# Kernel tuning notes

Hardware: AMD Instinct MI355X
Metric: run time of the kernel (lower is better)

Reference implementation:

```python
import jax, jax.numpy as jnp
import numpy as np
from jax import lax

EPS = 1e-5  # BatchNorm eps (torch default)


def _bn_relu_conv3x3_s2(x, bn_w, bn_b, bn_m, bn_v, w, b):
    # eval-mode BatchNorm2d -> ReLU -> conv3x3 stride 2 pad 1 (NCHW)
    inv = bn_w / jnp.sqrt(bn_v + EPS)
    y = x * inv[None, :, None, None] + (bn_b - bn_m * inv)[None, :, None, None]
    y = jax.nn.relu(y)
    y = lax.conv_general_dilated(y, w, window_strides=(2, 2),
                                 padding=((1, 1), (1, 1)),
                                 dimension_numbers=("NCHW", "OIHW", "NCHW"))
    return y + b[None, :, None, None]


def _avgpool2x2(x):
    B, C, H, W = x.shape
    return x.reshape(B, C, H // 2, 2, W // 2, 2).mean(axis=(3, 5))


def setup_inputs() -> dict:
    key = jax.random.key(0)
    ks = jax.random.split(key, 24)
    C, C3 = 128, 128 // 3
    d = {"x": jax.random.normal(ks[0], (8, C, 96, 96), jnp.float32)}
    for i, p in enumerate(["f", "g", "h"]):
        base = 1 + i * 6
        d[p + "_bn_w"] = jax.random.uniform(ks[base], (C,), jnp.float32, 0.5, 1.5)
        d[p + "_bn_b"] = jax.random.normal(ks[base + 1], (C,), jnp.float32) * 0.1
        d[p + "_bn_m"] = jax.random.normal(ks[base + 2], (C,), jnp.float32) * 0.1
        d[p + "_bn_v"] = jax.random.uniform(ks[base + 3], (C,), jnp.float32, 0.5, 1.5)
        d[p + "_w"] = jax.random.normal(ks[base + 4], (C, C, 3, 3), jnp.float32) * (1.0 / np.sqrt(9 * C))
        d[p + "_b"] = jax.random.normal(ks[base + 5], (C,), jnp.float32) * 0.01
    d["se_cw"] = jax.random.normal(ks[19], (C3, 2 * C), jnp.float32) * (1.0 / np.sqrt(2 * C))
    d["se_cb"] = jax.random.normal(ks[20], (C3,), jnp.float32) * 0.01
    d["se_uw"] = jax.random.normal(ks[21], (C, C3), jnp.float32) * (1.0 / np.sqrt(C3))
    d["se_ub"] = jax.random.normal(ks[22], (C,), jnp.float32) * 0.01
    d["gamma"] = jax.random.normal(ks[23], (1,), jnp.float32) * 0.5
    return d


def reference(x, f_bn_w, f_bn_b, f_bn_m, f_bn_v, f_w, f_b,
              g_bn_w, g_bn_b, g_bn_m, g_bn_v, g_w, g_b,
              h_bn_w, h_bn_b, h_bn_m, h_bn_v, h_w, h_b,
              se_cw, se_cb, se_uw, se_ub, gamma):
    B, C, H, W = x.shape
    left = _avgpool2x2(x)  # isPrimary=False branch -> [B,C,H/2,W/2]

    f = _bn_relu_conv3x3_s2(x, f_bn_w, f_bn_b, f_bn_m, f_bn_v, f_w, f_b)
    g = _bn_relu_conv3x3_s2(x, g_bn_w, g_bn_b, g_bn_m, g_bn_v, g_w, g_b)
    h = _bn_relu_conv3x3_s2(x, h_bn_w, h_bn_b, h_bn_m, h_bn_v, h_w, h_b)

    Ho, Wo = f.shape[2], f.shape[3]
    N = Ho * Wo
    ff = f.reshape(B, C, N)
    gg = g.reshape(B, C, N)
    hh = h.reshape(B, C, N)

    # s = softmax over last axis of f^T g : [B, N, N]
    scores = jnp.einsum("bcn,bcm->bnm", ff, gg)
    attn = jax.nn.softmax(scores, axis=2)
    s = jnp.einsum("bcn,bnm->bcm", hh, attn).reshape(B, C, Ho, Wo)
    s = gamma[0] * s

    # CompetitiveSE: global-avg x and s -> concat(2C) -> ReLU/1x1(C//3) -> ReLU/1x1(C)
    wx = x.mean(axis=(2, 3))          # [B, C]
    ws = s.mean(axis=(2, 3))          # [B, C]
    wcat = jnp.concatenate([wx, ws], axis=1)  # [B, 2C]
    se = jax.nn.relu(wcat) @ se_cw.T + se_cb
    se = jax.nn.relu(se) @ se_uw.T + se_ub    # [B, C]

    return (left + s) * (1.0 + se[:, :, None, None])
```

## Files before the change

kernel.cpp:

```cpp
#include <hip/hip_runtime.h>
#include <hip/hip_bf16.h>

#define B_   8
#define C_   128
#define H_   96
#define W_   96
#define HP_  98
#define HO_  48
#define N_   2304
#define K_CONV 1152
#define PLANE_IN  9216
#define TOT_OUT (B_*C_*N_)

typedef __attribute__((ext_vector_type(8))) short          s16x8;
typedef __attribute__((ext_vector_type(8))) unsigned short u16x8;
typedef __attribute__((ext_vector_type(4))) unsigned short u16x4;
typedef __attribute__((ext_vector_type(4))) float          f32x4;

#define SW(row, q)   (((row) << 6) + ((((q) ^ (((row) >> 1) & 3))) << 4))
#define SW8(row, q)  (((row) << 7) + ((((q) ^ ((row) & 7))) << 4))
#define SW16(row, q) (((row) << 8) + ((((q) ^ ((row) & 15))) << 4))

__device__ __forceinline__ ushort f2bf(float f) {
  __hip_bfloat16 h = __float2bfloat16(f);
  return *reinterpret_cast<ushort*>(&h);
}

__device__ __forceinline__ float block_reduce_sum_256(float v) {
  #pragma unroll
  for (int o = 32; o > 0; o >>= 1) v += __shfl_down(v, o, 64);
  __shared__ float r[4];
  int lane = threadIdx.x & 63, wv = threadIdx.x >> 6;
  if (lane == 0) r[wv] = v;
  __syncthreads();
  float s = 0.f;
  if (threadIdx.x == 0) s = r[0] + r[1] + r[2] + r[3];
  __syncthreads();
  return s;
}

__global__ void k_prep(const float* __restrict__ w0, const float* __restrict__ b0,
                       const float* __restrict__ m0, const float* __restrict__ v0,
                       const float* __restrict__ w1, const float* __restrict__ b1,
                       const float* __restrict__ m1, const float* __restrict__ v1,
                       const float* __restrict__ w2, const float* __restrict__ b2,
                       const float* __restrict__ m2, const float* __restrict__ v2,
                       float* __restrict__ inv, float* __restrict__ beta) {
  int p = blockIdx.x, c = threadIdx.x;
  const float* w = (p == 0 ? w0 : p == 1 ? w1 : w2);
  const float* bb = (p == 0 ? b0 : p == 1 ? b1 : b2);
  const float* m = (p == 0 ? m0 : p == 1 ? m1 : m2);
  const float* v = (p == 0 ? v0 : p == 1 ? v1 : v2);
  if (c < C_) {
    float iv = w[c] / sqrtf(v[c] + 1e-5f);
    inv[p * 128 + c] = iv;
    beta[p * 128 + c] = bb[c] - m[c] * iv;
  }
}

__global__ __launch_bounds__(256) void k_prep_w(const float* __restrict__ w0,
                                                const float* __restrict__ w1,
                                                const float* __restrict__ w2,
                                                ushort* __restrict__ o0,
                                                ushort* __restrict__ o1,
                                                ushort* __restrict__ o2) {
  int p = blockIdx.y;
  const float* w = (p == 0 ? w0 : p == 1 ? w1 : w2);
  ushort* wb = (p == 0 ? o0 : p == 1 ? o1 : o2);
  int id = blockIdx.x * 256 + threadIdx.x;
  if (id >= C_ * K_CONV) return;
  int co = id / K_CONV, rem = id - co * K_CONV;
  int tap = rem >> 7, ci = rem & 127;
  wb[id] = f2bf(w[co * K_CONV + ci * 9 + tap]);
}

__global__ __launch_bounds__(256) void k_prep_y(const float* __restrict__ x,
                                                const float* __restrict__ pinv,
                                                const float* __restrict__ pbeta,
                                                ushort* __restrict__ y0,
                                                ushort* __restrict__ y1,
                                                ushort* __restrict__ y2) {
  const int h1 = blockIdx.x, b = blockIdx.y, t = threadIdx.x;
  ushort* ys[3] = {y0 + (size_t)b * HP_ * HP_ * C_,
                   y1 + (size_t)b * HP_ * HP_ * C_,
                   y2 + (size_t)b * HP_ * HP_ * C_};
  u16x8 zer = (u16x8)0;
  if (h1 == 0 || h1 == HP_ - 1) {
    for (int p = 0; p < 3; ++p)
      for (int g = t; g < HP_ * C_ / 8; g += 256)
        *(u16x8*)(ys[p] + (size_t)h1 * HP_ * C_ + g * 8) = zer;
    return;
  }
  __shared__ float xs[128][97];
  const int h = h1 - 1;
  const float* xb = x + (size_t)b * C_ * PLANE_IN + h * W_;
  for (int id = t; id < 128 * 24; id += 256) {
    int ci = id / 24, w4 = id - ci * 24;
    float4 v = *(const float4*)(xb + (size_t)ci * PLANE_IN + w4 * 4);
    xs[ci][w4 * 4 + 0] = v.x; xs[ci][w4 * 4 + 1] = v.y;
    xs[ci][w4 * 4 + 2] = v.z; xs[ci][w4 * 4 + 3] = v.w;
  }
  __syncthreads();
  if (t < 32) {
    int side = t >> 4, cg = t & 15;
    for (int p = 0; p < 3; ++p)
      *(u16x8*)(ys[p] + ((size_t)h1 * HP_ + (side ? HP_ - 1 : 0)) * C_ + cg * 8) = zer;
  }
  for (int p = 0; p < 3; ++p) {
    const float* inv = pinv + p * 128;
    const float* bet = pbeta + p * 128;
    for (int g = t; g < 96 * 16; g += 256) {
      int wdx = g >> 4, cg = g & 15;
      u16x8 o;
      #pragma unroll
      for (int k = 0; k < 8; ++k) {
        int ci = cg * 8 + k;
        o[k] = f2bf(fmaxf(xs[ci][wdx] * inv[ci] + bet[ci], 0.f));
      }
      *(u16x8*)(ys[p] + ((size_t)h1 * HP_ + (wdx + 1)) * C_ + cg * 8) = o;
    }
  }
}

__global__ __launch_bounds__(256) void k_meanx(const float* __restrict__ x,
                                               float* __restrict__ wcat) {
  int bc = blockIdx.x;
  const float* p = x + (size_t)bc * PLANE_IN;
  float s = 0.f;
  for (int i = threadIdx.x; i < PLANE_IN; i += 256) s += p[i];
  s = block_reduce_sum_256(s);
  if (threadIdx.x == 0) {
    int b = bc >> 7, c = bc & 127;
    wcat[b * 256 + c] = fmaxf(s * (1.f / PLANE_IN), 0.f);
  }
}

__global__ __launch_bounds__(256) void k_conv3(
    const ushort* __restrict__ y0, const ushort* __restrict__ y1, const ushort* __restrict__ y2,
    const ushort* __restrict__ w0, const ushort* __restrict__ w1, const ushort* __restrict__ w2,
    const float* __restrict__ bi0, const float* __restrict__ bi1, const float* __restrict__ bi2,
    ushort* __restrict__ fo, ushort* __restrict__ go, ushort* __restrict__ ho) {
  __shared__ __align__(16) char smem[16384];
  char* As = smem;
  char* Bs = smem + 8192;
  const int br = blockIdx.y, b = blockIdx.z, n0 = blockIdx.x * 64;
  const int t = threadIdx.x, l = t & 63, w = t >> 6;
  const ushort* yb = (br == 0 ? y0 : br == 1 ? y1 : y2) + (size_t)b * HP_ * HP_ * C_;
  const ushort* wb = (br == 0 ? w0 : br == 1 ? w1 : w2);
  const float* bias = (br == 0 ? bi0 : br == 1 ? bi1 : bi2);
  const int pos = t >> 2, q = t & 3;
  const int n_glob = n0 + pos;
  const int oh = n_glob / HO_, ow = n_glob - oh * HO_;
  const int mh = (w & 1) * 64, nh = (w >> 1) * 32;
  f32x4 acc[4][2];
  #pragma unroll
  for (int i = 0; i < 4; ++i)
    #pragma unroll
    for (int j = 0; j < 2; ++j) acc[i][j] = (f32x4)0.f;

  for (int k0 = 0; k0 < K_CONV; k0 += 32) {
    int tap = k0 >> 7, ci0 = k0 & 127;
    int kh = tap / 3, kw = tap - kh * 3;
    #pragma unroll
    for (int g2 = 0; g2 < 2; ++g2) {
      int g = t + g2 * 256, row = g >> 2, qq = g & 3;
      u16x8 d = *(const u16x8*)(wb + row * K_CONV + k0 + qq * 8);
      *(u16x8*)(As + SW(row, qq)) = d;
    }
    {
      int h1 = 2 * oh + kh, w1 = 2 * ow + kw;
      u16x8 d = *(const u16x8*)(yb + ((size_t)h1 * HP_ + w1) * C_ + ci0 + q * 8);
      *(u16x8*)(Bs + SW(pos, q)) = d;
    }
    __syncthreads();
    s16x8 af[4], bf[2];
    #pragma unroll
    for (int i = 0; i < 4; ++i) {
      int r = mh + i * 16 + (l & 15);
      af[i] = *(const s16x8*)(As + SW(r, (l >> 4)));
    }
    #pragma unroll
    for (int j = 0; j < 2; ++j) {
      int r = nh + j * 16 + (l & 15);
      bf[j] = *(const s16x8*)(Bs + SW(r, (l >> 4)));
    }
    #pragma unroll
    for (int i = 0; i < 4; ++i)
      #pragma unroll
      for (int j = 0; j < 2; ++j)
        acc[i][j] = __builtin_amdgcn_mfma_f32_16x16x32_bf16(af[i], bf[j], acc[i][j], 0, 0, 0);
    __syncthreads();
  }

  if (br < 2) {
    ushort* out = (br == 0) ? fo : go;
    ushort* tb = (ushort*)smem;
    #pragma unroll
    for (int i = 0; i < 4; ++i) {
      int co4 = mh + i * 16 + (l >> 4) * 4;
      float4 bi = *(const float4*)&bias[co4];
      float bia[4] = {bi.x, bi.y, bi.z, bi.w};
      #pragma unroll
      for (int j = 0; j < 2; ++j) {
        int pp = nh + j * 16 + (l & 15);
        #pragma unroll
        for (int r = 0; r < 4; ++r)
          tb[pp * 128 + co4 + r] = f2bf(acc[i][j][r] + bia[r]);
      }
    }
    __syncthreads();
    #pragma unroll
    for (int it = 0; it < 4; ++it) {
      int g = t + it * 256;
      int row = g >> 4, gg = g & 15;
      u16x8 d = *(const u16x8*)(tb + row * 128 + gg * 8);
      *(u16x8*)(out + ((size_t)b * N_ + n0 + row) * C_ + gg * 8) = d;
    }
  } else {
    ushort* tb = (ushort*)smem;
    #pragma unroll
    for (int i = 0; i < 4; ++i) {
      int co4 = mh + i * 16 + (l >> 4) * 4;
      float4 bi = *(const float4*)&bias[co4];
      float bia[4] = {bi.x, bi.y, bi.z, bi.w};
      #pragma unroll
      for (int j = 0; j < 2; ++j) {
        int pp = nh + j * 16 + (l & 15);
        #pragma unroll
        for (int r = 0; r < 4; ++r)
          tb[(co4 + r) * 64 + pp] = f2bf(acc[i][j][r] + bia[r]);
      }
    }
    __syncthreads();
    for (int g = t; g < 1024; g += 256) {
      int co = g >> 3, off2 = (g & 7) * 8;
      u16x8 d = *(const u16x8*)(tb + co * 64 + off2);
      *(u16x8*)(ho + ((size_t)b * C_ + co) * N_ + n0 + off2) = d;
    }
  }
}

__global__ __launch_bounds__(256) void k_stats(const ushort* __restrict__ f,
                                               const ushort* __restrict__ g,
                                               float2* __restrict__ pstats) {
  __shared__ __align__(16) char smem[32768];
  char* fs = smem;
  char* gs = smem + 16384;
  const int blk = blockIdx.x;
  const int b = blk & 7, t2 = blk >> 3;
  const int n0 = (t2 % 36) * 64, mz = t2 / 36;
  const int t = threadIdx.x, l = t & 63, w = t >> 6, lo = l & 15, quad = l >> 4;
  const ushort* fb = f + (size_t)b * N_ * C_;
  const ushort* gb = g + (size_t)b * N_ * C_;
  #pragma unroll
  for (int it = 0; it < 4; ++it) {
    int G = t + it * 256, row = G >> 4, g16 = G & 15;
    *(u16x8*)(fs + SW16(row, g16)) = *(const u16x8*)(fb + (size_t)(n0 + row) * C_ + g16 * 8);
  }
  __syncthreads();
  s16x8 af[4];
  #pragma unroll
  for (int ks = 0; ks < 4; ++ks)
    af[ks] = *(const s16x8*)(fs + SW16(w * 16 + lo, ks * 4 + quad));
  float mloc[4], lloc[4];
  #pragma unroll
  for (int r = 0; r < 4; ++r) { mloc[r] = -1e30f; lloc[r] = 0.f; }
  const int m_beg = mz * 576;

  for (int i9 = 0; i9 < 9; ++i9) {
    int m0 = m_beg + i9 * 64;
    __syncthreads();
    #pragma unroll
    for (int it = 0; it < 4; ++it) {
      int G = t + it * 256, row = G >> 4, g16 = G & 15;
      *(u16x8*)(gs + SW16(row, g16)) = *(const u16x8*)(gb + (size_t)(m0 + row) * C_ + g16 * 8);
    }
    __syncthreads();
    f32x4 acc[4];
    #pragma unroll
    for (int j = 0; j < 4; ++j) acc[j] = (f32x4)0.f;
    #pragma unroll
    for (int ks = 0; ks < 4; ++ks)
      #pragma unroll
      for (int j = 0; j < 4; ++j) {
        s16x8 bf = *(const s16x8*)(gs + SW16(j * 16 + lo, ks * 4 + quad));
        acc[j] = __builtin_amdgcn_mfma_f32_16x16x32_bf16(af[ks], bf, acc[j], 0, 0, 0);
      }
    #pragma unroll
    for (int r = 0; r < 4; ++r) {
      float vmax = fmaxf(fmaxf(acc[0][r], acc[1][r]), fmaxf(acc[2][r], acc[3][r]));
      float mn = fmaxf(mloc[r], vmax);
      lloc[r] = lloc[r] * __expf(mloc[r] - mn) +
                __expf(acc[0][r] - mn) + __expf(acc[1][r] - mn) +
                __expf(acc[2][r] - mn) + __expf(acc[3][r] - mn);
      mloc[r] = mn;
    }
  }
  #pragma unroll
  for (int r = 0; r < 4; ++r) {
    #pragma unroll
    for (int o = 1; o < 16; o <<= 1) {
      float mo = __shfl_xor(mloc[r], o, 64);
      float lo2 = __shfl_xor(lloc[r], o, 64);
      float mn = fmaxf(mloc[r], mo);
      lloc[r] = lloc[r] * __expf(mloc[r] - mn) + lo2 * __expf(mo - mn);
      mloc[r] = mn;
    }
  }
  if (lo == 0) {
    #pragma unroll
    for (int r = 0; r < 4; ++r)
      pstats[((size_t)mz * B_ + b) * N_ + n0 + w * 16 + quad * 4 + r] =
          make_float2(mloc[r], lloc[r]);
  }
}

__global__ __launch_bounds__(256) void k_stats_red(const float2* __restrict__ p,
                                                   float2* __restrict__ stats) {
  int idx = blockIdx.x * 256 + threadIdx.x;
  if (idx >= B_ * N_) return;
  float mx = -1e30f, ls = 0.f;
  #pragma unroll
  for (int z = 0; z < 4; ++z) {
    float2 s = p[(size_t)z * B_ * N_ + idx];
    float mn = fmaxf(mx, s.x);
    ls = ls * __expf(mx - mn) + s.y * __expf(s.x - mn);
    mx = mn;
  }
  stats[idx] = make_float2(mx, ls);
}

__global__ __launch_bounds__(256) void k_attn_out(const ushort* __restrict__ f,
                                                  const ushort* __restrict__ g,
                                                  const ushort* __restrict__ h,
                                                  const float2* __restrict__ stats,
                                                  float* __restrict__ spart) {
  __shared__ __align__(16) char smem[35072];
  char* gs = smem;
  char* pTb = smem + 16384;
  const int blk = blockIdx.x;
  const int b = blk & 7, t2 = blk >> 3;
  const int m0 = (t2 % 36) * 64, nz = t2 / 36;
  const int t = threadIdx.x, l = t & 63, w = t >> 6, lo = l & 15, quad = l >> 4;
  const ushort* fb = f + (size_t)b * N_ * C_;
  const ushort* gb = g + (size_t)b * N_ * C_;
  const ushort* hb = h + (size_t)b * C_ * N_;
  const float2* stb = stats + (size_t)b * N_;
  #pragma unroll
  for (int it = 0; it < 4; ++it) {
    int G = t + it * 256, row = G >> 4, g16 = G & 15;
    *(u16x8*)(gs + SW16(row, g16)) = *(const u16x8*)(gb + (size_t)(m0 + row) * C_ + g16 * 8);
  }
  __syncthreads();
  f32x4 accs[2][4];
  #pragma unroll
  for (int i = 0; i < 2; ++i)
    #pragma unroll
    for (int j = 0; j < 4; ++j) accs[i][j] = (f32x4)0.f;
  const int n_beg = nz * 576;

  for (int i9 = 0; i9 < 9; ++i9) {
    int nb = n_beg + i9 * 64;
    char* pT = pTb + ((i9 & 1) << 13);
    s16x8 af[4], ah[2][2];
    #pragma unroll
    for (int ks = 0; ks < 4; ++ks)
      af[ks] = *(const s16x8*)(fb + (size_t)(nb + w * 16 + lo) * C_ + (ks * 4 + quad) * 8);
    #pragma unroll
    for (int i = 0; i < 2; ++i)
      #pragma unroll
      for (int ks = 0; ks < 2; ++ks)
        ah[i][ks] = *(const s16x8*)(hb + (size_t)((2 * w + i) * 16 + lo) * N_ + nb + (ks * 4 + quad) * 8);
    f32x4 sc[4];
    #pragma unroll
    for (int j = 0; j < 4; ++j) sc[j] = (f32x4)0.f;
    #pragma unroll
    for (int ks = 0; ks < 4; ++ks)
      #pragma unroll
      for (int j = 0; j < 4; ++j) {
        s16x8 bg = *(const s16x8*)(gs + SW16(j * 16 + lo, ks * 4 + quad));
        sc[j] = __builtin_amdgcn_mfma_f32_16x16x32_bf16(af[ks], bg, sc[j], 0, 0, 0);
      }
    float mxr[4], ilr[4];
    #pragma unroll
    for (int r = 0; r < 4; ++r) {
      float2 st = stb[nb + w * 16 + quad * 4 + r];
      mxr[r] = st.x; ilr[r] = 1.f / st.y;
    }
    const int nl = w * 16 + quad * 4;
    #pragma unroll
    for (int j = 0; j < 4; ++j) {
      u16x4 pv;
      #pragma unroll
      for (int r = 0; r < 4; ++r)
        pv[r] = f2bf(__expf(sc[j][r] - mxr[r]) * ilr[r]);
      *(u16x4*)(pT + SW8(j * 16 + lo, nl >> 3) + (nl & 7) * 2) = pv;
    }
    __syncthreads();
    #pragma unroll
    for (int ks = 0; ks < 2; ++ks)
      #pragma unroll
      for (int j = 0; j < 4; ++j) {
        s16x8 bp = *(const s16x8*)(pT + SW8(j * 16 + lo, ks * 4 + quad));
        accs[0][j] = __builtin_amdgcn_mfma_f32_16x16x32_bf16(ah[0][ks], bp, accs[0][j], 0, 0, 0);
        accs[1][j] = __builtin_amdgcn_mfma_f32_16x16x32_bf16(ah[1][ks], bp, accs[1][j], 0, 0, 0);
      }
  }
  __syncthreads();
  float* ss = (float*)smem;
  #pragma unroll
  for (int i = 0; i < 2; ++i) {
    int c0 = (2 * w + i) * 16 + quad * 4;
    #pragma unroll
    for (int j = 0; j < 4; ++j) {
      int m = j * 16 + lo;
      #pragma unroll
      for (int r = 0; r < 4; ++r)
        ss[(c0 + r) * 68 + m] = accs[i][j][r];
    }
  }
  __syncthreads();
  float* outp = spart + (size_t)nz * TOT_OUT + (size_t)b * C_ * N_ + m0;
  #pragma unroll
  for (int it = 0; it < 8; ++it) {
    int idx = t + it * 256;
    int c = idx >> 4, mq = idx & 15;
    float4 v = *(const float4*)&ss[c * 68 + mq * 4];
    *(float4*)&outp[(size_t)c * N_ + mq * 4] = v;
  }
}

__global__ __launch_bounds__(256) void k_sred(const float* __restrict__ spart,
                                              const float* __restrict__ gammap,
                                              float* __restrict__ sbuf) {
  int idx = blockIdx.x * 256 + threadIdx.x;
  if (idx >= TOT_OUT) return;
  float s = spart[idx] + spart[(size_t)TOT_OUT + idx] +
            spart[2 * (size_t)TOT_OUT + idx] + spart[3 * (size_t)TOT_OUT + idx];
  sbuf[idx] = gammap[0] * s;
}

__global__ __launch_bounds__(256) void k_means(const float* __restrict__ s,
                                               float* __restrict__ wcat) {
  int bc = blockIdx.x;
  const float* p = s + (size_t)bc * N_;
  float sm = 0.f;
  for (int i = threadIdx.x; i < N_; i += 256) sm += p[i];
  sm = block_reduce_sum_256(sm);
  if (threadIdx.x == 0) {
    int b = bc >> 7, c = bc & 127;
    wcat[b * 256 + 128 + c] = fmaxf(sm * (1.f / N_), 0.f);
  }
}

__global__ __launch_bounds__(128) void k_se(const float* __restrict__ wcat,
                                            const float* __restrict__ cw,
                                            const float* __restrict__ cb,
                                            const float* __restrict__ uw,
                                            const float* __restrict__ ub,
                                            float* __restrict__ se) {
  const int b = blockIdx.x, t = threadIdx.x;
  __shared__ float wc[256];
  __shared__ float s1[42];
  wc[t] = wcat[b * 256 + t];
  wc[128 + t] = wcat[b * 256 + 128 + t];
  __syncthreads();
  if (t < 42) {
    float a = cb[t];
    const float* r = cw + (size_t)t * 256;
    for (int k = 0; k < 256; ++k) a += wc[k] * r[k];
    s1[t] = fmaxf(a, 0.f);
  }
  __syncthreads();
  {
    float a = ub[t];
    const float* r = uw + (size_t)t * 42;
    for (int j = 0; j < 42; ++j) a += s1[j] * r[j];
    se[b * 128 + t] = a;
  }
}

__global__ __launch_bounds__(256) void k_final(const float* __restrict__ x,
                                               const float* __restrict__ s,
                                               const float* __restrict__ se,
                                               float* __restrict__ out) {
  int idx = blockIdx.x * 256 + threadIdx.x;
  if (idx >= TOT_OUT) return;
  int m  = idx % N_;
  int bc = idx / N_;
  int oh = m / HO_, ow = m - oh * HO_;
  const float* xp = x + (size_t)bc * PLANE_IN;
  int ih = oh * 2, iw = ow * 2;
  float l = 0.25f * (xp[ih * W_ + iw] + xp[ih * W_ + iw + 1] +
                     xp[(ih + 1) * W_ + iw] + xp[(ih + 1) * W_ + iw + 1]);
  out[idx] = (l + s[idx]) * (1.f + se[bc]);
}

extern "C" void kernel_launch(void* const* d_in, const int* in_sizes, int n_in,
                              void* d_out, int out_size, void* d_ws, size_t ws_size,
                              hipStream_t stream) {
  (void)in_sizes; (void)n_in; (void)out_size; (void)ws_size;
  const float* x    = (const float*)d_in[0];
  const float* bnw[3] = {(const float*)d_in[1],  (const float*)d_in[7],  (const float*)d_in[13]};
  const float* bnb[3] = {(const float*)d_in[2],  (const float*)d_in[8],  (const float*)d_in[14]};
  const float* bnm[3] = {(const float*)d_in[3],  (const float*)d_in[9],  (const float*)d_in[15]};
  const float* bnv[3] = {(const float*)d_in[4],  (const float*)d_in[10], (const float*)d_in[16]};
  const float* cw_[3] = {(const float*)d_in[5],  (const float*)d_in[11], (const float*)d_in[17]};
  const float* cbb[3] = {(const float*)d_in[6],  (const float*)d_in[12], (const float*)d_in[18]};
  const float* secw = (const float*)d_in[19];
  const float* secb = (const float*)d_in[20];
  const float* seuw = (const float*)d_in[21];
  const float* seub = (const float*)d_in[22];
  const float* gamma = (const float*)d_in[23];
  float* out = (float*)d_out;

  char* ws = (char*)d_ws;
  size_t off = 0;
  auto alloc = [&](size_t bytes) -> char* {
    char* p = ws + off;
    off = (off + bytes + 255) & ~(size_t)255;
    return p;
  };
  ushort* yp[3];
  for (int p = 0; p < 3; ++p) yp[p] = (ushort*)alloc((size_t)B_ * HP_ * HP_ * C_ * 2);
  ushort* wb[3];
  for (int p = 0; p < 3; ++p) wb[p] = (ushort*)alloc((size_t)C_ * K_CONV * 2);
  ushort* fbuf = (ushort*)alloc((size_t)B_ * N_ * C_ * 2);
  ushort* gbuf = (ushort*)alloc((size_t)B_ * N_ * C_ * 2);
  ushort* hbuf = (ushort*)alloc((size_t)B_ * C_ * N_ * 2);
  float2* pstats = (float2*)alloc((size_t)4 * B_ * N_ * 8);
  float2* stats  = (float2*)alloc((size_t)B_ * N_ * 8);
  float*  spart = (float*)alloc((size_t)4 * TOT_OUT * 4);
  float*  sbuf = (float*)alloc((size_t)TOT_OUT * 4);
  float*  wcat = (float*)alloc(B_ * 256 * 4);
  float*  sebuf = (float*)alloc(B_ * 128 * 4);
  float*  pinv  = (float*)alloc(3 * 128 * 4);
  float*  pbeta = (float*)alloc(3 * 128 * 4);

  k_prep<<<3, 128, 0, stream>>>(bnw[0], bnb[0], bnm[0], bnv[0],
                                bnw[1], bnb[1], bnm[1], bnv[1],
                                bnw[2], bnb[2], bnm[2], bnv[2], pinv, pbeta);
  k_prep_w<<<dim3((C_ * K_CONV + 255) / 256, 3), 256, 0, stream>>>(
      cw_[0], cw_[1], cw_[2], wb[0], wb[1], wb[2]);
  k_prep_y<<<dim3(HP_, B_), 256, 0, stream>>>(x, pinv, pbeta, yp[0], yp[1], yp[2]);
  k_meanx<<<B_ * C_, 256, 0, stream>>>(x, wcat);

  k_conv3<<<dim3(N_ / 64, 3, B_), 256, 0, stream>>>(yp[0], yp[1], yp[2],
                                                    wb[0], wb[1], wb[2],
                                                    cbb[0], cbb[1], cbb[2],
                                                    fbuf, gbuf, hbuf);

  k_stats<<<1152, 256, 0, stream>>>(fbuf, gbuf, pstats);
  k_stats_red<<<(B_ * N_ + 255) / 256, 256, 0, stream>>>(pstats, stats);
  k_attn_out<<<1152, 256, 0, stream>>>(fbuf, gbuf, hbuf, stats, spart);
  k_sred<<<(TOT_OUT + 255) / 256, 256, 0, stream>>>(spart, gamma, sbuf);

  k_means<<<B_ * C_, 256, 0, stream>>>(sbuf, wcat);
  k_se<<<B_, 128, 0, stream>>>(wcat, secw, secb, seuw, seub, sebuf);

  k_final<<<(TOT_OUT + 255) / 256, 256, 0, stream>>>(x, sbuf, sebuf, out);
}
```

Before: 304.5 us.

## Drop LDS staging in attention kernels, per-wave tiles, fuse reduce with means

k_stats and k_attn_out now read f and g MFMA fragments straight from global memory instead of staging them through swizzled LDS, which removes most __syncthreads. k_attn_out is restructured so each wave owns its own 16 m columns, keeps its probability tile in a private LDS slice and accumulates all 128 channels in registers, writing results to global without an LDS transpose. The partial-sum reduction and the per-channel mean are fused into one kernel, saving a full read of sbuf. The trade-off is that operand reuse across waves now relies on L1/L2 caching rather than LDS, and the direct scalar stores to spart are less coalesced than before.

Measured after the change: 469.2 us. 1.54x slower.

```diff
diff --git a/kernel.cpp b/kernel.cpp
--- a/kernel.cpp
+++ b/kernel.cpp
@@ -18,7 +18,6 @@
 typedef __attribute__((ext_vector_type(4))) float          f32x4;
 
 #define SW(row, q)   (((row) << 6) + ((((q) ^ (((row) >> 1) & 3))) << 4))
-#define SW8(row, q)  (((row) << 7) + ((((q) ^ ((row) & 7))) << 4))
 #define SW16(row, q) (((row) << 8) + ((((q) ^ ((row) & 15))) << 4))
 
 __device__ __forceinline__ ushort f2bf(float f) {
@@ -243,25 +242,16 @@
 __global__ __launch_bounds__(256) void k_stats(const ushort* __restrict__ f,
                                                const ushort* __restrict__ g,
                                                float2* __restrict__ pstats) {
-  __shared__ __align__(16) char smem[32768];
-  char* fs = smem;
-  char* gs = smem + 16384;
   const int blk = blockIdx.x;
   const int b = blk & 7, t2 = blk >> 3;
   const int n0 = (t2 % 36) * 64, mz = t2 / 36;
   const int t = threadIdx.x, l = t & 63, w = t >> 6, lo = l & 15, quad = l >> 4;
   const ushort* fb = f + (size_t)b * N_ * C_;
   const ushort* gb = g + (size_t)b * N_ * C_;
-  #pragma unroll
-  for (int it = 0; it < 4; ++it) {
-    int G = t + it * 256, row = G >> 4, g16 = G & 15;
-    *(u16x8*)(fs + SW16(row, g16)) = *(const u16x8*)(fb + (size_t)(n0 + row) * C_ + g16 * 8);
-  }
-  __syncthreads();
   s16x8 af[4];
   #pragma unroll
   for (int ks = 0; ks < 4; ++ks)
-    af[ks] = *(const s16x8*)(fs + SW16(w * 16 + lo, ks * 4 + quad));
+    af[ks] = *(const s16x8*)(fb + (size_t)(n0 + w * 16 + lo) * C_ + (ks * 4 + quad) * 8);
   float mloc[4], lloc[4];
   #pragma unroll
   for (int r = 0; r < 4; ++r) { mloc[r] = -1e30f; lloc[r] = 0.f; }
@@ -269,23 +259,21 @@
 
   for (int i9 = 0; i9 < 9; ++i9) {
     int m0 = m_beg + i9 * 64;
-    __syncthreads();
-    #pragma unroll
-    for (int it = 0; it < 4; ++it) {
-      int G = t + it * 256, row = G >> 4, g16 = G & 15;
-      *(u16x8*)(gs + SW16(row, g16)) = *(const u16x8*)(gb + (size_t)(m0 + row) * C_ + g16 * 8);
-    }
-    __syncthreads();
     f32x4 acc[4];
     #pragma unroll
     for (int j = 0; j < 4; ++j) acc[j] = (f32x4)0.f;
     #pragma unroll
-    for (int ks = 0; ks < 4; ++ks)
-      #pragma unroll
-      for (int j = 0; j < 4; ++j) {
-        s16x8 bf = *(const s16x8*)(gs + SW16(j * 16 + lo, ks * 4 + quad));
-        acc[j] = __builtin_amdgcn_mfma_f32_16x16x32_bf16(af[ks], bf, acc[j], 0, 0, 0);
-      }
+    for (int j = 0; j < 4; ++j) {
+      const ushort* gr = gb + (size_t)(m0 + j * 16 + lo) * C_ + quad * 8;
+      s16x8 b0 = *(const s16x8*)(gr);
+      s16x8 b1 = *(const s16x8*)(gr + 32);
+      s16x8 b2 = *(const s16x8*)(gr + 64);
+      s16x8 b3 = *(const s16x8*)(gr + 96);
+      acc[j] = __builtin_amdgcn_mfma_f32_16x16x32_bf16(af[0], b0, acc[j], 0, 0, 0);
+      acc[j] = __builtin_amdgcn_mfma_f32_16x16x32_bf16(af[1], b1, acc[j], 0, 0, 0);
+      acc[j] = __builtin_amdgcn_mfma_f32_16x16x32_bf16(af[2], b2, acc[j], 0, 0, 0);
+      acc[j] = __builtin_amdgcn_mfma_f32_16x16x32_bf16(af[3], b3, acc[j], 0, 0, 0);
+    }
     #pragma unroll
     for (int r = 0; r < 4; ++r) {
       float vmax = fmaxf(fmaxf(acc[0][r], acc[1][r]), fmaxf(acc[2][r], acc[3][r]));
@@ -335,9 +323,7 @@
                                                   const ushort* __restrict__ h,
                                                   const float2* __restrict__ stats,
                                                   float* __restrict__ spart) {
-  __shared__ __align__(16) char smem[35072];
-  char* gs = smem;
-  char* pTb = smem + 16384;
+  __shared__ __align__(16) ushort pw[4][16 * 72];
   const int blk = blockIdx.x;
   const int b = blk & 7, t2 = blk >> 3;
   const int m0 = (t2 % 36) * 64, nz = t2 / 36;
@@ -346,106 +332,78 @@
   const ushort* gb = g + (size_t)b * N_ * C_;
   const ushort* hb = h + (size_t)b * C_ * N_;
   const float2* stb = stats + (size_t)b * N_;
-  #pragma unroll
-  for (int it = 0; it < 4; ++it) {
-    int G = t + it * 256, row = G >> 4, g16 = G & 15;
-    *(u16x8*)(gs + SW16(row, g16)) = *(const u16x8*)(gb + (size_t)(m0 + row) * C_ + g16 * 8);
-  }
-  __syncthreads();
-  f32x4 accs[2][4];
-  #pragma unroll
-  for (int i = 0; i < 2; ++i)
-    #pragma unroll
-    for (int j = 0; j < 4; ++j) accs[i][j] = (f32x4)0.f;
+  const int mw = m0 + w * 16;
+  ushort* pwv = &pw[w][0];
+  s16x8 bg[4];
+  #pragma unroll
+  for (int ks = 0; ks < 4; ++ks)
+    bg[ks] = *(const s16x8*)(gb + (size_t)(mw + lo) * C_ + (ks * 4 + quad) * 8);
+  f32x4 acc[8];
+  #pragma unroll
+  for (int i2 = 0; i2 < 8; ++i2) acc[i2] = (f32x4)0.f;
   const int n_beg = nz * 576;
 
   for (int i9 = 0; i9 < 9; ++i9) {
     int nb = n_beg + i9 * 64;
-    char* pT = pTb + ((i9 & 1) << 13);
-    s16x8 af[4], ah[2][2];
-    #pragma unroll
-    for (int ks = 0; ks < 4; ++ks)
-      af[ks] = *(const s16x8*)(fb + (size_t)(nb + w * 16 + lo) * C_ + (ks * 4 + quad) * 8);
-    #pragma unroll
-    for (int i = 0; i < 2; ++i)
-      #pragma unroll
-      for (int ks = 0; ks < 2; ++ks)
-        ah[i][ks] = *(const s16x8*)(hb + (size_t)((2 * w + i) * 16 + lo) * N_ + nb + (ks * 4 + quad) * 8);
-    f32x4 sc[4];
-    #pragma unroll
-    for (int j = 0; j < 4; ++j) sc[j] = (f32x4)0.f;
-    #pragma unroll
-    for (int ks = 0; ks < 4; ++ks)
-      #pragma unroll
-      for (int j = 0; j < 4; ++j) {
-        s16x8 bg = *(const s16x8*)(gs + SW16(j * 16 + lo, ks * 4 + quad));
-        sc[j] = __builtin_amdgcn_mfma_f32_16x16x32_bf16(af[ks], bg, sc[j], 0, 0, 0);
-      }
-    float mxr[4], ilr[4];
-    #pragma unroll
-    for (int r = 0; r < 4; ++r) {
-      float2 st = stb[nb + w * 16 + quad * 4 + r];
-      mxr[r] = st.x; ilr[r] = 1.f / st.y;
-    }
-    const int nl = w * 16 + quad * 4;
-    #pragma unroll
-    for (int j = 0; j < 4; ++j) {
+    #pragma unroll
+    for (int i = 0; i < 4; ++i) {
+      const ushort* fr = fb + (size_t)(nb + i * 16 + lo) * C_ + quad * 8;
+      s16x8 a0 = *(const s16x8*)(fr);
+      s16x8 a1 = *(const s16x8*)(fr + 32);
+      s16x8 a2 = *(const s16x8*)(fr + 64);
+      s16x8 a3 = *(const s16x8*)(fr + 96);
+      f32x4 sc = (f32x4)0.f;
+      sc = __builtin_amdgcn_mfma_f32_16x16x32_bf16(a0, bg[0], sc, 0, 0, 0);
+      sc = __builtin_amdgcn_mfma_f32_16x16x32_bf16(a1, bg[1], sc, 0, 0, 0);
+      sc = __builtin_amdgcn_mfma_f32_16x16x32_bf16(a2, bg[2], sc, 0, 0, 0);
+      sc = __builtin_amdgcn_mfma_f32_16x16x32_bf16(a3, bg[3], sc, 0, 0, 0);
+      float4 q1 = *(const float4*)&stb[nb + i * 16 + quad * 4];
+      float4 q2 = *(const float4*)&stb[nb + i * 16 + quad * 4 + 2];
       u16x4 pv;
-      #pragma unroll
-      for (int r = 0; r < 4; ++r)
-        pv[r] = f2bf(__expf(sc[j][r] - mxr[r]) * ilr[r]);
-      *(u16x4*)(pT + SW8(j * 16 + lo, nl >> 3) + (nl & 7) * 2) = pv;
-    }
-    __syncthreads();
-    #pragma unroll
-    for (int ks = 0; ks < 2; ++ks)
-      #pragma unroll
-      for (int j = 0; j < 4; ++j) {
-        s16x8 bp = *(const s16x8*)(pT + SW8(j * 16 + lo, ks * 4 + quad));
-        accs[0][j] = __builtin_amdgcn_mfma_f32_16x16x32_bf16(ah[0][ks], bp, accs[0][j], 0, 0, 0);
-        accs[1][j] = __builtin_amdgcn_mfma_f32_16x16x32_bf16(ah[1][ks], bp, accs[1][j], 0, 0, 0);
-      }
-  }
-  __syncthreads();
-  float* ss = (float*)smem;
-  #pragma unroll
-  for (int i = 0; i < 2; ++i) {
-    int c0 = (2 * w + i) * 16 + quad * 4;
-    #pragma unroll
-    for (int j = 0; j < 4; ++j) {
-      int m = j * 16 + lo;
-      #pragma unroll
-      for (int r = 0; r < 4; ++r)
-        ss[(c0 + r) * 68 + m] = accs[i][j][r];
-    }
-  }
-  __syncthreads();
-  float* outp = spart + (size_t)nz * TOT_OUT + (size_t)b * C_ * N_ + m0;
-  #pragma unroll
-  for (int it = 0; it < 8; ++it) {
-    int idx = t + it * 256;
-    int c = idx >> 4, mq = idx & 15;
-    float4 v = *(const float4*)&ss[c * 68 + mq * 4];
-    *(float4*)&outp[(size_t)c * N_ + mq * 4] = v;
-  }
-}
-
-__global__ __launch_bounds__(256) void k_sred(const float* __restrict__ spart,
-                                              const float* __restrict__ gammap,
-                                              float* __restrict__ sbuf) {
-  int idx = blockIdx.x * 256 + threadIdx.x;
-  if (idx >= TOT_OUT) return;
-  float s = spart[idx] + spart[(size_t)TOT_OUT + idx] +
-            spart[2 * (size_t)TOT_OUT + idx] + spart[3 * (size_t)TOT_OUT + idx];
-  sbuf[idx] = gammap[0] * s;
-}
-
-__global__ __launch_bounds__(256) void k_means(const float* __restrict__ s,
+      pv[0] = f2bf(__expf(sc[0] - q1.x) / q1.y);
+      pv[1] = f2bf(__expf(sc[1] - q1.z) / q1.w);
+      pv[2] = f2bf(__expf(sc[2] - q2.x) / q2.y);
+      pv[3] = f2bf(__expf(sc[3] - q2.z) / q2.w);
+      *(u16x4*)(pwv + lo * 72 + i * 16 + quad * 4) = pv;
+    }
+    s16x8 bp0 = *(const s16x8*)(pwv + lo * 72 + quad * 8);
+    s16x8 bp1 = *(const s16x8*)(pwv + lo * 72 + 32 + quad * 8);
+    #pragma unroll
+    for (int i2 = 0; i2 < 8; ++i2) {
+      const ushort* hr = hb + (size_t)(i2 * 16 + lo) * N_ + nb + quad * 8;
+      s16x8 ah0 = *(const s16x8*)(hr);
+      s16x8 ah1 = *(const s16x8*)(hr + 32);
+      acc[i2] = __builtin_amdgcn_mfma_f32_16x16x32_bf16(ah0, bp0, acc[i2], 0, 0, 0);
+      acc[i2] = __builtin_amdgcn_mfma_f32_16x16x32_bf16(ah1, bp1, acc[i2], 0, 0, 0);
+    }
+  }
+  float* outp = spart + (size_t)nz * TOT_OUT + (size_t)b * C_ * N_;
+  #pragma unroll
+  for (int i2 = 0; i2 < 8; ++i2) {
+    #pragma unroll
+    for (int r = 0; r < 4; ++r)
+      outp[(size_t)(i2 * 16 + quad * 4 + r) * N_ + mw + lo] = acc[i2][r];
+  }
+}
+
+__global__ __launch_bounds__(256) void k_sredm(const float* __restrict__ spart,
+                                               const float* __restrict__ gammap,
+                                               float* __restrict__ sbuf,
                                                float* __restrict__ wcat) {
-  int bc = blockIdx.x;
-  const float* p = s + (size_t)bc * N_;
+  const int bc = blockIdx.x;
+  const float gv = gammap[0];
+  const size_t row = (size_t)bc * N_;
   float sm = 0.f;
-  for (int i = threadIdx.x; i < N_; i += 256) sm += p[i];
+  for (int i4 = threadIdx.x; i4 < N_ / 4; i4 += 256) {
+    float4 a = *(const float4*)&spart[row + i4 * 4];
+    float4 c = *(const float4*)&spart[(size_t)TOT_OUT + row + i4 * 4];
+    float4 d = *(const float4*)&spart[2 * (size_t)TOT_OUT + row + i4 * 4];
+    float4 e = *(const float4*)&spart[3 * (size_t)TOT_OUT + row + i4 * 4];
+    float4 o = make_float4(gv * (a.x + c.x + d.x + e.x), gv * (a.y + c.y + d.y + e.y),
+                           gv * (a.z + c.z + d.z + e.z), gv * (a.w + c.w + d.w + e.w));
+    *(float4*)&sbuf[row + i4 * 4] = o;
+    sm += o.x + o.y + o.z + o.w;
+  }
   sm = block_reduce_sum_256(sm);
   if (threadIdx.x == 0) {
     int b = bc >> 7, c = bc & 127;
@@ -553,9 +511,8 @@
   k_stats<<<1152, 256, 0, stream>>>(fbuf, gbuf, pstats);
   k_stats_red<<<(B_ * N_ + 255) / 256, 256, 0, stream>>>(pstats, stats);
   k_attn_out<<<1152, 256, 0, stream>>>(fbuf, gbuf, hbuf, stats, spart);
-  k_sred<<<(TOT_OUT + 255) / 256, 256, 0, stream>>>(spart, gamma, sbuf);
-
-  k_means<<<B_ * C_, 256, 0, stream>>>(sbuf, wcat);
+  k_sredm<<<B_ * C_, 256, 0, stream>>>(spart, gamma, sbuf, wcat);
+
   k_se<<<B_, 128, 0, stream>>>(wcat, secw, secb, seuw, seub, sebuf);
 
   k_final<<<(TOT_OUT + 255) / 256, 256, 0, stream>>>(x, sbuf, sebuf, out);
```
